# Optimization experiments

Measured on AMD Instinct MI355X. Metric: run time of the kernel, lower is better.

Reference implementation:

```python
import jax, jax.numpy as jnp
import numpy as np

N, E, B = 50000, 800000, 8
DN = DE = DU = DO = 32   # node/edge/global/out feature dims
H = 64                   # MLP hidden dim


def _linear_params(key, din, dout):
    kw, kb = jax.random.split(key)
    W = jax.random.normal(kw, (din, dout), dtype=jnp.float32) * 0.02
    b = jax.random.normal(kb, (dout,), dtype=jnp.float32) * 0.02
    return W, b


def setup_inputs() -> dict:
    key = jax.random.key(0)
    ks = jax.random.split(key, 13)
    edge_feat = jax.random.normal(ks[0], (E, DE), dtype=jnp.float32)
    node_feat = jax.random.normal(ks[1], (N, DN), dtype=jnp.float32)
    g_repr = jax.random.normal(ks[2], (B, DU), dtype=jnp.float32)
    src = jax.random.randint(ks[3], (E,), 0, N)
    dst = jax.random.randint(ks[4], (E,), 0, N)
    node2graph = jnp.sort(jax.random.randint(ks[5], (N,), 0, B))
    edge2graph = jnp.sort(jax.random.randint(ks[6], (E,), 0, B))
    W_e1, b_e1 = _linear_params(ks[7], DE + 2 * DN + DU, H)   # fc_edge
    W_e2, b_e2 = _linear_params(ks[8], H, DO)                 # fc_edge2
    W_n1, b_n1 = _linear_params(ks[9], DN + DO + DU, H)       # fc_node
    W_n2, b_n2 = _linear_params(ks[10], H, DO)                # fc_node2
    W_u1, b_u1 = _linear_params(ks[11], 2 * DO + DU, H)       # fc_u
    W_u2, b_u2 = _linear_params(ks[12], H, DO)                # fc_u2
    return dict(edge_feat=edge_feat, node_feat=node_feat, g_repr=g_repr,
                src=src, dst=dst, node2graph=node2graph, edge2graph=edge2graph,
                W_e1=W_e1, b_e1=b_e1, W_e2=W_e2, b_e2=b_e2,
                W_n1=W_n1, b_n1=b_n1, W_n2=W_n2, b_n2=b_n2,
                W_u1=W_u1, b_u1=b_u1, W_u2=W_u2, b_u2=b_u2)


def reference(edge_feat, node_feat, g_repr, src, dst, node2graph, edge2graph,
              W_e1, b_e1, W_e2, b_e2, W_n1, b_n1, W_n2, b_n2,
              W_u1, b_u1, W_u2, b_u2):
    relu = jax.nn.relu
    # --- edge update: concat(edge, src node, dst node, per-edge global) -> MLP ---
    e_inp = jnp.concatenate([edge_feat, node_feat[src], node_feat[dst],
                             g_repr[edge2graph]], axis=-1)          # [E, DE+2DN+DU]
    e_out = relu(e_inp @ W_e1 + b_e1) @ W_e2 + b_e2                 # [E, DO]
    # --- message passing: sum updated edge feats into dst nodes ---
    h = jax.ops.segment_sum(e_out, dst, num_segments=N)             # [N, DO]
    # --- node update: concat(node, h, per-node global) -> MLP (F.relu in source) ---
    n_inp = jnp.concatenate([node_feat, h, g_repr[node2graph]], axis=-1)
    n_out = relu(n_inp @ W_n1 + b_n1) @ W_n2 + b_n2                 # [N, DO]
    # --- global update: per-graph sums of edge/node feats + old global ---
    e_comb = jax.ops.segment_sum(e_out, edge2graph, num_segments=B)  # [B, DO]
    n_comb = jax.ops.segment_sum(n_out, node2graph, num_segments=B)  # [B, DO]
    u_inp = jnp.concatenate([n_comb, e_comb, g_repr], axis=-1)
    g_out = relu(u_inp @ W_u1 + b_u1) @ W_u2 + b_u2                  # [B, DO]
    return (e_out, n_out, g_out)
```

## Files before the change

kernel.cpp:

```cpp
#include <hip/hip_runtime.h>
#include <hip/hip_bf16.h>

typedef __bf16 bf16x8 __attribute__((ext_vector_type(8)));
typedef float f32x4 __attribute__((ext_vector_type(4)));
typedef unsigned short ushort_t;

static __device__ __forceinline__ bf16x8 cvt8(const float4& a, const float4& b) {
    bf16x8 r;
    r[0] = (__bf16)a.x; r[1] = (__bf16)a.y; r[2] = (__bf16)a.z; r[3] = (__bf16)a.w;
    r[4] = (__bf16)b.x; r[5] = (__bf16)b.y; r[6] = (__bf16)b.z; r[7] = (__bf16)b.w;
    return r;
}
static __device__ __forceinline__ bf16x8 load8(const float* p) {
    const float4* q = (const float4*)p;
    float4 a = q[0], b = q[1];
    return cvt8(a, b);
}

__global__ void zero_ws(float4* p, int n4) {
    int idx = blockIdx.x * blockDim.x + threadIdx.x;
    int stride = gridDim.x * blockDim.x;
    float4 z = make_float4(0.f, 0.f, 0.f, 0.f);
    for (; idx < n4; idx += stride) p[idx] = z;
}

__global__ void pack_weights(const float* __restrict__ We1, const float* __restrict__ We2,
                             const float* __restrict__ Wn1, const float* __restrict__ Wn2,
                             ushort_t* __restrict__ wf_e1, ushort_t* __restrict__ wf_e2,
                             ushort_t* __restrict__ wf_n1, ushort_t* __restrict__ wf_n2) {
    int tid = threadIdx.x;
    for (int idx = tid; idx < 16 * 512; idx += 256) {
        int f = idx >> 9, rem = idx & 511, l = rem >> 3, i = rem & 7;
        int t = f >> 2, s = f & 3;
        int k = s * 32 + (l >> 4) * 8 + i, n = t * 16 + (l & 15);
        wf_e1[idx] = __builtin_bit_cast(ushort_t, (__bf16)We1[k * 64 + n]);
    }
    for (int idx = tid; idx < 4 * 512; idx += 256) {
        int f = idx >> 9, rem = idx & 511, l = rem >> 3, i = rem & 7;
        int t = f >> 1, s = f & 1;
        int k = s * 32 + (l >> 4) * 8 + i, n = t * 16 + (l & 15);
        wf_e2[idx] = __builtin_bit_cast(ushort_t, (__bf16)We2[k * 32 + n]);
    }
    for (int idx = tid; idx < 12 * 512; idx += 256) {
        int f = idx >> 9, rem = idx & 511, l = rem >> 3, i = rem & 7;
        int t = f / 3, s = f - t * 3;
        int k = s * 32 + (l >> 4) * 8 + i, n = t * 16 + (l & 15);
        wf_n1[idx] = __builtin_bit_cast(ushort_t, (__bf16)Wn1[k * 64 + n]);
    }
    for (int idx = tid; idx < 4 * 512; idx += 256) {
        int f = idx >> 9, rem = idx & 511, l = rem >> 3, i = rem & 7;
        int t = f >> 1, s = f & 1;
        int k = s * 32 + (l >> 4) * 8 + i, n = t * 16 + (l & 15);
        wf_n2[idx] = __builtin_bit_cast(ushort_t, (__bf16)Wn2[k * 32 + n]);
    }
}

__launch_bounds__(256)
__global__ void edge_kernel(
    const float* __restrict__ edge_feat, const float* __restrict__ node_feat,
    const float* __restrict__ g_repr, const int* __restrict__ src,
    const int* __restrict__ dst, const int* __restrict__ e2g,
    const ushort_t* __restrict__ wf1, const ushort_t* __restrict__ wf2,
    const float* __restrict__ b1, const float* __restrict__ b2,
    float* __restrict__ e_out, float* __restrict__ h_node,
    float* __restrict__ e_comb, int E) {
    __shared__ float lds_h[4][16][68];
    __shared__ float lds_ec[256];
    int tid = threadIdx.x;
    lds_ec[tid] = 0.f;
    __syncthreads();
    int lane = tid & 63, wid = tid >> 6;
    int lo = lane & 15, kg = lane >> 4;

    const bf16x8* pf1 = (const bf16x8*)wf1;
    const bf16x8* pf2 = (const bf16x8*)wf2;
    bf16x8 w1[4][4], w2[2][2];
#pragma unroll
    for (int t = 0; t < 4; ++t)
#pragma unroll
        for (int s = 0; s < 4; ++s) w1[t][s] = pf1[(t * 4 + s) * 64 + lane];
#pragma unroll
    for (int t = 0; t < 2; ++t)
#pragma unroll
        for (int s = 0; s < 2; ++s) w2[t][s] = pf2[(t * 2 + s) * 64 + lane];
    float bias1[4], bias2[2];
#pragma unroll
    for (int t = 0; t < 4; ++t) bias1[t] = b1[t * 16 + lo];
#pragma unroll
    for (int t = 0; t < 2; ++t) bias2[t] = b2[t * 16 + lo];

    int nTiles = E >> 4;
    int gw = gridDim.x * 4;
    for (int tile = blockIdx.x * 4 + wid; tile < nTiles; tile += gw) {
        int m0 = tile << 4;
        int arow = m0 + lo;
        int si = src[arow], di = dst[arow], gi = e2g[arow];
        bf16x8 a[4];
        a[0] = load8(edge_feat + (size_t)arow * 32 + kg * 8);
        a[1] = load8(node_feat + (size_t)si * 32 + kg * 8);
        a[2] = load8(node_feat + (size_t)di * 32 + kg * 8);
        a[3] = load8(g_repr + (size_t)gi * 32 + kg * 8);
#pragma unroll
        for (int t = 0; t < 4; ++t) {
            f32x4 acc = {0.f, 0.f, 0.f, 0.f};
#pragma unroll
            for (int s = 0; s < 4; ++s)
                acc = __builtin_amdgcn_mfma_f32_16x16x32_bf16(a[s], w1[t][s], acc, 0, 0, 0);
            int col = t * 16 + lo;
#pragma unroll
            for (int r = 0; r < 4; ++r)
                lds_h[wid][kg * 4 + r][col] = fmaxf(acc[r] + bias1[t], 0.f);
        }
        bf16x8 ha[2];
#pragma unroll
        for (int s = 0; s < 2; ++s) {
            const float* p = &lds_h[wid][lo][s * 32 + kg * 8];
            const float4* q = (const float4*)p;
            ha[s] = cvt8(q[0], q[1]);
        }
        int drow[4], grow[4];
#pragma unroll
        for (int r = 0; r < 4; ++r) {
            int em = m0 + kg * 4 + r;
            drow[r] = dst[em];
            grow[r] = e2g[em];
        }
#pragma unroll
        for (int t = 0; t < 2; ++t) {
            f32x4 acc = {0.f, 0.f, 0.f, 0.f};
#pragma unroll
            for (int s = 0; s < 2; ++s)
                acc = __builtin_amdgcn_mfma_f32_16x16x32_bf16(ha[s], w2[t][s], acc, 0, 0, 0);
            int col = t * 16 + lo;
#pragma unroll
            for (int r = 0; r < 4; ++r) {
                float v = acc[r] + bias2[t];
                int em = m0 + kg * 4 + r;
                e_out[(size_t)em * 32 + col] = v;
                atomicAdd(&h_node[(size_t)drow[r] * 32 + col], v);
                atomicAdd(&lds_ec[grow[r] * 32 + col], v);
            }
        }
    }
    __syncthreads();
    atomicAdd(&e_comb[tid], lds_ec[tid]);
}

__launch_bounds__(256)
__global__ void node_kernel(
    const float* __restrict__ node_feat, const float* __restrict__ g_repr,
    const int* __restrict__ n2g, const float* __restrict__ h_node,
    const ushort_t* __restrict__ wf1, const ushort_t* __restrict__ wf2,
    const float* __restrict__ b1, const float* __restrict__ b2,
    float* __restrict__ n_out, float* __restrict__ n_comb, int N) {
    __shared__ float lds_h[4][16][68];
    __shared__ float lds_nc[256];
    int tid = threadIdx.x;
    lds_nc[tid] = 0.f;
    __syncthreads();
    int lane = tid & 63, wid = tid >> 6;
    int lo = lane & 15, kg = lane >> 4;

    const bf16x8* pf1 = (const bf16x8*)wf1;
    const bf16x8* pf2 = (const bf16x8*)wf2;
    bf16x8 w1[4][3], w2[2][2];
#pragma unroll
    for (int t = 0; t < 4; ++t)
#pragma unroll
        for (int s = 0; s < 3; ++s) w1[t][s] = pf1[(t * 3 + s) * 64 + lane];
#pragma unroll
    for (int t = 0; t < 2; ++t)
#pragma unroll
        for (int s = 0; s < 2; ++s) w2[t][s] = pf2[(t * 2 + s) * 64 + lane];
    float bias1[4], bias2[2];
#pragma unroll
    for (int t = 0; t < 4; ++t) bias1[t] = b1[t * 16 + lo];
#pragma unroll
    for (int t = 0; t < 2; ++t) bias2[t] = b2[t * 16 + lo];

    int nTiles = N >> 4;
    int gw = gridDim.x * 4;
    for (int tile = blockIdx.x * 4 + wid; tile < nTiles; tile += gw) {
        int m0 = tile << 4;
        int arow = m0 + lo;
        int gi = n2g[arow];
        bf16x8 a[3];
        a[0] = load8(node_feat + (size_t)arow * 32 + kg * 8);
        a[1] = load8(h_node + (size_t)arow * 32 + kg * 8);
        a[2] = load8(g_repr + (size_t)gi * 32 + kg * 8);
#pragma unroll
        for (int t = 0; t < 4; ++t) {
            f32x4 acc = {0.f, 0.f, 0.f, 0.f};
#pragma unroll
            for (int s = 0; s < 3; ++s)
                acc = __builtin_amdgcn_mfma_f32_16x16x32_bf16(a[s], w1[t][s], acc, 0, 0, 0);
            int col = t * 16 + lo;
#pragma unroll
            for (int r = 0; r < 4; ++r)
                lds_h[wid][kg * 4 + r][col] = fmaxf(acc[r] + bias1[t], 0.f);
        }
        bf16x8 ha[2];
#pragma unroll
        for (int s = 0; s < 2; ++s) {
            const float* p = &lds_h[wid][lo][s * 32 + kg * 8];
            const float4* q = (const float4*)p;
            ha[s] = cvt8(q[0], q[1]);
        }
        int grow[4];
#pragma unroll
        for (int r = 0; r < 4; ++r) grow[r] = n2g[m0 + kg * 4 + r];
#pragma unroll
        for (int t = 0; t < 2; ++t) {
            f32x4 acc = {0.f, 0.f, 0.f, 0.f};
#pragma unroll
            for (int s = 0; s < 2; ++s)
                acc = __builtin_amdgcn_mfma_f32_16x16x32_bf16(ha[s], w2[t][s], acc, 0, 0, 0);
            int col = t * 16 + lo;
#pragma unroll
            for (int r = 0; r < 4; ++r) {
                float v = acc[r] + bias2[t];
                int em = m0 + kg * 4 + r;
                n_out[(size_t)em * 32 + col] = v;
                atomicAdd(&lds_nc[grow[r] * 32 + col], v);
            }
        }
    }
    __syncthreads();
    atomicAdd(&n_comb[tid], lds_nc[tid]);
}

__global__ void global_kernel(const float* __restrict__ g_repr, const float* __restrict__ e_comb,
                              const float* __restrict__ n_comb, const float* __restrict__ Wu1,
                              const float* __restrict__ bu1, const float* __restrict__ Wu2,
                              const float* __restrict__ bu2, float* __restrict__ g_out) {
    __shared__ float u[8][96];
    __shared__ float hh[8][64];
    int tid = threadIdx.x;
    {
        int i = tid >> 5, c = tid & 31;
        u[i][c] = n_comb[tid];
        u[i][32 + c] = e_comb[tid];
        u[i][64 + c] = g_repr[tid];
    }
    __syncthreads();
    for (int idx = tid; idx < 512; idx += 256) {
        int i = idx >> 6, j = idx & 63;
        float s = bu1[j];
        for (int k = 0; k < 96; ++k) s += u[i][k] * Wu1[k * 64 + j];
        hh[i][j] = fmaxf(s, 0.f);
    }
    __syncthreads();
    {
        int i = tid >> 5, c = tid & 31;
        float s = bu2[c];
        for (int j = 0; j < 64; ++j) s += hh[i][j] * Wu2[j * 32 + c];
        g_out[tid] = s;
    }
}

extern "C" void kernel_launch(void* const* d_in, const int* in_sizes, int n_in,
                              void* d_out, int out_size, void* d_ws, size_t ws_size,
                              hipStream_t stream) {
    const float* edge_feat = (const float*)d_in[0];
    const float* node_feat = (const float*)d_in[1];
    const float* g_repr = (const float*)d_in[2];
    const int* src = (const int*)d_in[3];
    const int* dst = (const int*)d_in[4];
    const int* n2g = (const int*)d_in[5];
    const int* e2g = (const int*)d_in[6];
    const float* We1 = (const float*)d_in[7];
    const float* be1 = (const float*)d_in[8];
    const float* We2 = (const float*)d_in[9];
    const float* be2 = (const float*)d_in[10];
    const float* Wn1 = (const float*)d_in[11];
    const float* bn1 = (const float*)d_in[12];
    const float* Wn2 = (const float*)d_in[13];
    const float* bn2 = (const float*)d_in[14];
    const float* Wu1 = (const float*)d_in[15];
    const float* bu1 = (const float*)d_in[16];
    const float* Wu2 = (const float*)d_in[17];
    const float* bu2 = (const float*)d_in[18];

    int E = in_sizes[3];
    int N = in_sizes[1] / 32;

    float* out = (float*)d_out;
    float* e_out = out;
    float* n_out = out + (size_t)E * 32;
    float* g_out = out + (size_t)(E + N) * 32;

    char* ws = (char*)d_ws;
    float* h_node = (float*)ws;
    float* e_comb = (float*)(ws + (size_t)N * 32 * 4);
    float* n_comb = e_comb + 256;
    ushort_t* wf_e1 = (ushort_t*)(n_comb + 256);
    ushort_t* wf_e2 = wf_e1 + 8192;
    ushort_t* wf_n1 = wf_e2 + 2048;
    ushort_t* wf_n2 = wf_n1 + 6144;

    int n4 = (N * 32 + 512) / 4;
    zero_ws<<<512, 256, 0, stream>>>((float4*)ws, n4);
    pack_weights<<<1, 256, 0, stream>>>(We1, We2, Wn1, Wn2, wf_e1, wf_e2, wf_n1, wf_n2);
    edge_kernel<<<1280, 256, 0, stream>>>(edge_feat, node_feat, g_repr, src, dst, e2g,
                                          wf_e1, wf_e2, be1, be2, e_out, h_node, e_comb, E);
    node_kernel<<<256, 256, 0, stream>>>(node_feat, g_repr, n2g, h_node,
                                         wf_n1, wf_n2, bn1, bn2, n_out, n_comb, N);
    global_kernel<<<1, 256, 0, stream>>>(g_repr, e_comb, n_comb, Wu1, bu1, Wu2, bu2, g_out);
}
```

Before: 374.0 us.

## Privatize node aggregation buffers per XCD with workgroup-scope atomics

Each XCD gets its own copy of the h_node scatter buffer and the per-graph sum buffers, selected by reading the hardware XCC_ID register. Atomics into these copies use workgroup-scope relaxed adds, so they can resolve in that XCD's L2 rather than as device-coherent atomics. The node kernel and the global kernel then sum the eight copies. Grid sizes for the edge and node kernels also grow. The price is eight times the zeroing and read traffic for h_node, plus reliance on the memory-scope semantics and on the workspace being large enough, with a fallback to the old path otherwise.

```diff
diff --git a/kernel.cpp b/kernel.cpp
--- a/kernel.cpp
+++ b/kernel.cpp
@@ -4,6 +4,8 @@
 typedef __bf16 bf16x8 __attribute__((ext_vector_type(8)));
 typedef float f32x4 __attribute__((ext_vector_type(4)));
 typedef unsigned short ushort_t;
+
+#define NXCD 8
 
 static __device__ __forceinline__ bf16x8 cvt8(const float4& a, const float4& b) {
     bf16x8 r;
@@ -15,6 +17,18 @@
     const float4* q = (const float4*)p;
     float4 a = q[0], b = q[1];
     return cvt8(a, b);
+}
+static __device__ __forceinline__ int xcc_id() {
+    int x;
+    asm volatile("s_getreg_b32 %0, hwreg(HW_REG_XCC_ID)" : "=s"(x));
+    return x & (NXCD - 1);
+}
+template <bool PRIV>
+static __device__ __forceinline__ void atomAddF(float* p, float v) {
+    if constexpr (PRIV)
+        __hip_atomic_fetch_add(p, v, __ATOMIC_RELAXED, __HIP_MEMORY_SCOPE_WORKGROUP);
+    else
+        atomicAdd(p, v);
 }
 
 __global__ void zero_ws(float4* p, int n4) {
@@ -55,6 +69,7 @@
     }
 }
 
+template <bool PRIV>
 __launch_bounds__(256)
 __global__ void edge_kernel(
     const float* __restrict__ edge_feat, const float* __restrict__ node_feat,
@@ -62,8 +77,8 @@
     const int* __restrict__ dst, const int* __restrict__ e2g,
     const ushort_t* __restrict__ wf1, const ushort_t* __restrict__ wf2,
     const float* __restrict__ b1, const float* __restrict__ b2,
-    float* __restrict__ e_out, float* __restrict__ h_node,
-    float* __restrict__ e_comb, int E) {
+    float* __restrict__ e_out, float* __restrict__ h_priv,
+    float* __restrict__ e_comb_priv, int E, int N) {
     __shared__ float lds_h[4][16][68];
     __shared__ float lds_ec[256];
     int tid = threadIdx.x;
@@ -71,6 +86,10 @@
     __syncthreads();
     int lane = tid & 63, wid = tid >> 6;
     int lo = lane & 15, kg = lane >> 4;
+
+    int xcd = PRIV ? xcc_id() : 0;
+    float* hbase = h_priv + (size_t)xcd * N * 32;
+    float* ecbase = e_comb_priv + xcd * 256;
 
     const bf16x8* pf1 = (const bf16x8*)wf1;
     const bf16x8* pf2 = (const bf16x8*)wf2;
@@ -137,22 +156,23 @@
                 float v = acc[r] + bias2[t];
                 int em = m0 + kg * 4 + r;
                 e_out[(size_t)em * 32 + col] = v;
-                atomicAdd(&h_node[(size_t)drow[r] * 32 + col], v);
+                atomAddF<PRIV>(&hbase[(size_t)drow[r] * 32 + col], v);
                 atomicAdd(&lds_ec[grow[r] * 32 + col], v);
             }
         }
     }
     __syncthreads();
-    atomicAdd(&e_comb[tid], lds_ec[tid]);
-}
-
+    atomAddF<PRIV>(&ecbase[tid], lds_ec[tid]);
+}
+
+template <bool PRIV>
 __launch_bounds__(256)
 __global__ void node_kernel(
     const float* __restrict__ node_feat, const float* __restrict__ g_repr,
-    const int* __restrict__ n2g, const float* __restrict__ h_node,
+    const int* __restrict__ n2g, const float* __restrict__ h_priv,
     const ushort_t* __restrict__ wf1, const ushort_t* __restrict__ wf2,
     const float* __restrict__ b1, const float* __restrict__ b2,
-    float* __restrict__ n_out, float* __restrict__ n_comb, int N) {
+    float* __restrict__ n_out, float* __restrict__ n_comb_priv, int N, int ncopies) {
     __shared__ float lds_h[4][16][68];
     __shared__ float lds_nc[256];
     int tid = threadIdx.x;
@@ -160,6 +180,9 @@
     __syncthreads();
     int lane = tid & 63, wid = tid >> 6;
     int lo = lane & 15, kg = lane >> 4;
+
+    int xcd = PRIV ? xcc_id() : 0;
+    float* ncbase = n_comb_priv + xcd * 256;
 
     const bf16x8* pf1 = (const bf16x8*)wf1;
     const bf16x8* pf2 = (const bf16x8*)wf2;
@@ -186,7 +209,17 @@
         int gi = n2g[arow];
         bf16x8 a[3];
         a[0] = load8(node_feat + (size_t)arow * 32 + kg * 8);
-        a[1] = load8(h_node + (size_t)arow * 32 + kg * 8);
+        {
+            float4 s0 = make_float4(0.f, 0.f, 0.f, 0.f), s1 = s0;
+            for (int c = 0; c < ncopies; ++c) {
+                const float4* q = (const float4*)(h_priv + (size_t)c * N * 32 +
+                                                  (size_t)arow * 32 + kg * 8);
+                float4 u0 = q[0], u1 = q[1];
+                s0.x += u0.x; s0.y += u0.y; s0.z += u0.z; s0.w += u0.w;
+                s1.x += u1.x; s1.y += u1.y; s1.z += u1.z; s1.w += u1.w;
+            }
+            a[1] = cvt8(s0, s1);
+        }
         a[2] = load8(g_repr + (size_t)gi * 32 + kg * 8);
 #pragma unroll
         for (int t = 0; t < 4; ++t) {
@@ -226,20 +259,25 @@
         }
     }
     __syncthreads();
-    atomicAdd(&n_comb[tid], lds_nc[tid]);
-}
-
-__global__ void global_kernel(const float* __restrict__ g_repr, const float* __restrict__ e_comb,
-                              const float* __restrict__ n_comb, const float* __restrict__ Wu1,
+    atomAddF<PRIV>(&ncbase[tid], lds_nc[tid]);
+}
+
+__global__ void global_kernel(const float* __restrict__ g_repr, const float* __restrict__ e_comb_priv,
+                              const float* __restrict__ n_comb_priv, const float* __restrict__ Wu1,
                               const float* __restrict__ bu1, const float* __restrict__ Wu2,
-                              const float* __restrict__ bu2, float* __restrict__ g_out) {
+                              const float* __restrict__ bu2, float* __restrict__ g_out, int ncopies) {
     __shared__ float u[8][96];
     __shared__ float hh[8][64];
     int tid = threadIdx.x;
     {
         int i = tid >> 5, c = tid & 31;
-        u[i][c] = n_comb[tid];
-        u[i][32 + c] = e_comb[tid];
+        float en = 0.f, ee = 0.f;
+        for (int x = 0; x < ncopies; ++x) {
+            en += n_comb_priv[x * 256 + tid];
+            ee += e_comb_priv[x * 256 + tid];
+        }
+        u[i][c] = en;
+        u[i][32 + c] = ee;
         u[i][64 + c] = g_repr[tid];
     }
     __syncthreads();
@@ -289,21 +327,33 @@
     float* n_out = out + (size_t)E * 32;
     float* g_out = out + (size_t)(E + N) * 32;
 
+    size_t need = ((size_t)NXCD * N * 32 + 2 * NXCD * 256 + 32768) * 4;
+    bool priv = ws_size >= need;
+    int ncopies = priv ? NXCD : 1;
+    size_t hElems = (size_t)ncopies * N * 32;
+
     char* ws = (char*)d_ws;
-    float* h_node = (float*)ws;
-    float* e_comb = (float*)(ws + (size_t)N * 32 * 4);
-    float* n_comb = e_comb + 256;
-    ushort_t* wf_e1 = (ushort_t*)(n_comb + 256);
+    float* h_priv = (float*)ws;
+    float* e_comb = h_priv + hElems;
+    float* n_comb = e_comb + ncopies * 256;
+    ushort_t* wf_e1 = (ushort_t*)(n_comb + ncopies * 256);
     ushort_t* wf_e2 = wf_e1 + 8192;
     ushort_t* wf_n1 = wf_e2 + 2048;
     ushort_t* wf_n2 = wf_n1 + 6144;
 
-    int n4 = (N * 32 + 512) / 4;
-    zero_ws<<<512, 256, 0, stream>>>((float4*)ws, n4);
+    int n4 = (int)((hElems + 2 * (size_t)ncopies * 256) / 4);
+    zero_ws<<<2048, 256, 0, stream>>>((float4*)ws, n4);
     pack_weights<<<1, 256, 0, stream>>>(We1, We2, Wn1, Wn2, wf_e1, wf_e2, wf_n1, wf_n2);
-    edge_kernel<<<1280, 256, 0, stream>>>(edge_feat, node_feat, g_repr, src, dst, e2g,
-                                          wf_e1, wf_e2, be1, be2, e_out, h_node, e_comb, E);
-    node_kernel<<<256, 256, 0, stream>>>(node_feat, g_repr, n2g, h_node,
-                                         wf_n1, wf_n2, bn1, bn2, n_out, n_comb, N);
-    global_kernel<<<1, 256, 0, stream>>>(g_repr, e_comb, n_comb, Wu1, bu1, Wu2, bu2, g_out);
-}
+    if (priv) {
+        edge_kernel<true><<<2048, 256, 0, stream>>>(edge_feat, node_feat, g_repr, src, dst, e2g,
+                                                    wf_e1, wf_e2, be1, be2, e_out, h_priv, e_comb, E, N);
+        node_kernel<true><<<800, 256, 0, stream>>>(node_feat, g_repr, n2g, h_priv,
+                                                   wf_n1, wf_n2, bn1, bn2, n_out, n_comb, N, ncopies);
+    } else {
+        edge_kernel<false><<<2048, 256, 0, stream>>>(edge_feat, node_feat, g_repr, src, dst, e2g,
+                                                     wf_e1, wf_e2, be1, be2, e_out, h_priv, e_comb, E, N);
+        node_kernel<false><<<800, 256, 0, stream>>>(node_feat, g_repr, n2g, h_priv,
+                                                    wf_n1, wf_n2, bn1, bn2, n_out, n_comb, N, ncopies);
+    }
+    global_kernel<<<1, 256, 0, stream>>>(g_repr, e_comb, n_comb, Wu1, bu1, Wu2, bu2, g_out, ncopies);
+}
```

After: 385.1 us. 3.0% more time.

## Replace atomic scatter of edge outputs with CSR-based segmented gather

Applied to the files above, without the earlier changes.

Builds a dst-sorted CSR index (histogram, single-block prefix scan, atomic fill) and computes the per-node sum with a gather kernel that reads e_out by edge id, instead of float atomics from the edge kernel. This removes the heavy global float atomic traffic into h_node and the need to zero it. It adds several extra launches, a serial single-block scan, integer atomics over all edges, and a random-access reread of e_out. Grid sizes for the edge and node kernels are also raised.

```diff
diff --git a/kernel.cpp b/kernel.cpp
--- a/kernel.cpp
+++ b/kernel.cpp
@@ -17,11 +17,58 @@
     return cvt8(a, b);
 }
 
-__global__ void zero_ws(float4* p, int n4) {
+__global__ void zero_ws(int* cnt, float* combs, int N) {
     int idx = blockIdx.x * blockDim.x + threadIdx.x;
     int stride = gridDim.x * blockDim.x;
-    float4 z = make_float4(0.f, 0.f, 0.f, 0.f);
-    for (; idx < n4; idx += stride) p[idx] = z;
+    for (int i = idx; i < N; i += stride) cnt[i] = 0;
+    if (idx < 512) combs[idx] = 0.f;
+}
+
+__global__ void hist_kernel(const int* __restrict__ dst, int* __restrict__ cnt, int E) {
+    int idx = blockIdx.x * blockDim.x + threadIdx.x;
+    int stride = gridDim.x * blockDim.x;
+    for (int e = idx; e < E; e += stride) atomicAdd(&cnt[dst[e]], 1);
+}
+
+__global__ void scan_kernel(const int* __restrict__ cnt, int* __restrict__ row_start,
+                            int* __restrict__ cursor, int N) {
+    __shared__ int lds[1024];
+    __shared__ int carry;
+    int tid = threadIdx.x;
+    if (tid == 0) carry = 0;
+    __syncthreads();
+    for (int base = 0; base < N; base += 1024) {
+        int i = base + tid;
+        int v = (i < N) ? cnt[i] : 0;
+        lds[tid] = v;
+        __syncthreads();
+        for (int off = 1; off < 1024; off <<= 1) {
+            int t = (tid >= off) ? lds[tid - off] : 0;
+            __syncthreads();
+            lds[tid] += t;
+            __syncthreads();
+        }
+        int incl = lds[tid];
+        int excl = incl - v;
+        if (i < N) {
+            row_start[i] = carry + excl;
+            cursor[i] = carry + excl;
+        }
+        __syncthreads();
+        if (tid == 1023) carry += lds[1023];
+        __syncthreads();
+    }
+    if (tid == 0) row_start[N] = carry;
+}
+
+__global__ void fill_kernel(const int* __restrict__ dst, int* __restrict__ cursor,
+                            int* __restrict__ eid, int E) {
+    int idx = blockIdx.x * blockDim.x + threadIdx.x;
+    int stride = gridDim.x * blockDim.x;
+    for (int e = idx; e < E; e += stride) {
+        int p = atomicAdd(&cursor[dst[e]], 1);
+        eid[p] = e;
+    }
 }
 
 __global__ void pack_weights(const float* __restrict__ We1, const float* __restrict__ We2,
@@ -62,8 +109,7 @@
     const int* __restrict__ dst, const int* __restrict__ e2g,
     const ushort_t* __restrict__ wf1, const ushort_t* __restrict__ wf2,
     const float* __restrict__ b1, const float* __restrict__ b2,
-    float* __restrict__ e_out, float* __restrict__ h_node,
-    float* __restrict__ e_comb, int E) {
+    float* __restrict__ e_out, float* __restrict__ e_comb, int E) {
     __shared__ float lds_h[4][16][68];
     __shared__ float lds_ec[256];
     int tid = threadIdx.x;
@@ -118,13 +164,9 @@
             const float4* q = (const float4*)p;
             ha[s] = cvt8(q[0], q[1]);
         }
-        int drow[4], grow[4];
-#pragma unroll
-        for (int r = 0; r < 4; ++r) {
-            int em = m0 + kg * 4 + r;
-            drow[r] = dst[em];
-            grow[r] = e2g[em];
-        }
+        int grow[4];
+#pragma unroll
+        for (int r = 0; r < 4; ++r) grow[r] = e2g[m0 + kg * 4 + r];
 #pragma unroll
         for (int t = 0; t < 2; ++t) {
             f32x4 acc = {0.f, 0.f, 0.f, 0.f};
@@ -137,19 +179,33 @@
                 float v = acc[r] + bias2[t];
                 int em = m0 + kg * 4 + r;
                 e_out[(size_t)em * 32 + col] = v;
-                atomicAdd(&h_node[(size_t)drow[r] * 32 + col], v);
                 atomicAdd(&lds_ec[grow[r] * 32 + col], v);
             }
         }
     }
     __syncthreads();
     atomicAdd(&e_comb[tid], lds_ec[tid]);
+}
+
+__launch_bounds__(256)
+__global__ void h_build(const float* __restrict__ e_out, const int* __restrict__ eid,
+                        const int* __restrict__ row_start, float* __restrict__ h, int N) {
+    int w = (blockIdx.x * blockDim.x + threadIdx.x) >> 6;
+    if (w >= N) return;
+    int lane = threadIdx.x & 63;
+    int half = lane >> 5, col = lane & 31;
+    int s = row_start[w], e = row_start[w + 1];
+    float acc = 0.f;
+    for (int j = s + half; j < e; j += 2)
+        acc += e_out[(size_t)eid[j] * 32 + col];
+    acc += __shfl_xor(acc, 32, 64);
+    if (half == 0) h[(size_t)w * 32 + col] = acc;
 }
 
 __launch_bounds__(256)
 __global__ void node_kernel(
     const float* __restrict__ node_feat, const float* __restrict__ g_repr,
-    const int* __restrict__ n2g, const float* __restrict__ h_node,
+    const int* __restrict__ n2g, const float* __restrict__ h,
     const ushort_t* __restrict__ wf1, const ushort_t* __restrict__ wf2,
     const float* __restrict__ b1, const float* __restrict__ b2,
     float* __restrict__ n_out, float* __restrict__ n_comb, int N) {
@@ -186,7 +242,7 @@
         int gi = n2g[arow];
         bf16x8 a[3];
         a[0] = load8(node_feat + (size_t)arow * 32 + kg * 8);
-        a[1] = load8(h_node + (size_t)arow * 32 + kg * 8);
+        a[1] = load8(h + (size_t)arow * 32 + kg * 8);
         a[2] = load8(g_repr + (size_t)gi * 32 + kg * 8);
 #pragma unroll
         for (int t = 0; t < 4; ++t) {
@@ -290,20 +346,27 @@
     float* g_out = out + (size_t)(E + N) * 32;
 
     char* ws = (char*)d_ws;
-    float* h_node = (float*)ws;
-    float* e_comb = (float*)(ws + (size_t)N * 32 * 4);
+    int* cnt = (int*)ws;
+    int* row_start = cnt + N;
+    int* cursor = row_start + N + 1;
+    int* eid = cursor + N;
+    float* h = (float*)(eid + E);
+    float* e_comb = h + (size_t)N * 32;
     float* n_comb = e_comb + 256;
     ushort_t* wf_e1 = (ushort_t*)(n_comb + 256);
     ushort_t* wf_e2 = wf_e1 + 8192;
     ushort_t* wf_n1 = wf_e2 + 2048;
     ushort_t* wf_n2 = wf_n1 + 6144;
 
-    int n4 = (N * 32 + 512) / 4;
-    zero_ws<<<512, 256, 0, stream>>>((float4*)ws, n4);
+    zero_ws<<<256, 256, 0, stream>>>(cnt, e_comb, N);
     pack_weights<<<1, 256, 0, stream>>>(We1, We2, Wn1, Wn2, wf_e1, wf_e2, wf_n1, wf_n2);
-    edge_kernel<<<1280, 256, 0, stream>>>(edge_feat, node_feat, g_repr, src, dst, e2g,
-                                          wf_e1, wf_e2, be1, be2, e_out, h_node, e_comb, E);
-    node_kernel<<<256, 256, 0, stream>>>(node_feat, g_repr, n2g, h_node,
+    hist_kernel<<<1024, 256, 0, stream>>>(dst, cnt, E);
+    scan_kernel<<<1, 1024, 0, stream>>>(cnt, row_start, cursor, N);
+    fill_kernel<<<1024, 256, 0, stream>>>(dst, cursor, eid, E);
+    edge_kernel<<<2048, 256, 0, stream>>>(edge_feat, node_feat, g_repr, src, dst, e2g,
+                                          wf_e1, wf_e2, be1, be2, e_out, e_comb, E);
+    h_build<<<(N + 3) / 4, 256, 0, stream>>>(e_out, eid, row_start, h, N);
+    node_kernel<<<800, 256, 0, stream>>>(node_feat, g_repr, n2g, h,
                                          wf_n1, wf_n2, bn1, bn2, n_out, n_comb, N);
     global_kernel<<<1, 256, 0, stream>>>(g_repr, e_comb, n_comb, Wu1, bu1, Wu2, bu2, g_out);
 }
```

After: 611.0 us. 63.4% more time.
